# Performance work log

Hardware: AMD Instinct MI355X
Metric: run time of the kernel (lower is better)

Reference implementation:

```python
import jax, jax.numpy as jnp
import numpy as np

L = 32768   # sequence length
H = 256     # dim_ssm_io
P = 128     # effective state dim = dim_ssm_state // 2 (conj_sym=True)
DT_MIN, DT_MAX = 0.001, 0.1


def setup_inputs() -> dict:
    key = jax.random.key(0)
    kB, kC, kD, kstep, ku = jax.random.split(key, 5)
    n = jnp.arange(P, dtype=jnp.float32)
    # s4d_inv initialization: Lambda = -0.5 + 1j * (P/pi) * (P/(2n+1) - 1)
    Lambda_re = -0.5 * jnp.ones((P,), dtype=jnp.float32)
    Lambda_im = (P / np.pi) * (P / (2.0 * n + 1.0) - 1.0)
    # lecun_normal over fan_in, then / sqrt(2) for conj_sym real/imag split
    B = jax.random.normal(kB, (P, H, 2), dtype=jnp.float32) / jnp.sqrt(2.0 * H)
    C = jax.random.normal(kC, (H, P, 2), dtype=jnp.float32) / jnp.sqrt(2.0 * P)
    D = jax.random.normal(kD, (H,), dtype=jnp.float32)
    log_step = (jax.random.uniform(kstep, (P,), dtype=jnp.float32)
                * (jnp.log(DT_MAX) - jnp.log(DT_MIN)) + jnp.log(DT_MIN))
    input_sequence = jax.random.normal(ku, (L, H), dtype=jnp.float32)
    return {
        "Lambda_re": Lambda_re, "Lambda_im": Lambda_im,
        "B": B, "C": C, "D": D, "log_step": log_step,
        "input_sequence": input_sequence,
    }


def reference(Lambda_re, Lambda_im, B, C, D, log_step, input_sequence):
    # assemble complex params (conj_sym path)
    Lam = Lambda_re + 1j * Lambda_im              # (P,)
    B_tilde = B[..., 0] + 1j * B[..., 1]          # (P, H)
    C_tilde = C[..., 0] + 1j * C[..., 1]          # (H, P)
    step = jnp.exp(log_step)                      # (P,)  step_rescale = 1.0
    # ZOH discretization
    Lambda_bar = jnp.exp(Lam * step)              # (P,)
    B_bar = ((Lambda_bar - 1.0) / Lam)[:, None] * B_tilde  # (P, H)
    # input projection: Bu[l] = B_bar @ u[l]
    Bu = jnp.einsum("lh,ph->lp", input_sequence.astype(B_bar.dtype), B_bar)  # (L, P)
    Lam_elems = jnp.broadcast_to(Lambda_bar, (input_sequence.shape[0], Lambda_bar.shape[0]))

    def lin_op(q_i, q_j):
        A_i, b_i = q_i
        A_j, b_j = q_j
        return (A_j * A_i, A_j * b_i + b_j)

    _, xs = jax.lax.associative_scan(lin_op, (Lam_elems, Bu))  # (L, P) complex
    # output projection with conj symmetry: 2 * Re(C_tilde @ x)
    ys = 2.0 * jnp.einsum("lp,hp->lh", xs, C_tilde).real       # (L, H)
    return ys + D * input_sequence
```

## Files before the change

kernel.cpp:

```cpp
#include <hip/hip_runtime.h>
#include <math.h>

#define L_SEQ   32768
#define H_DIM   256
#define P_DIM   128
#define P2      256
#define NBLK    512
#define ROWS    64
#define TPB     512
#define NSEG    64
#define CPS     8

#define WS_LB    0
#define WS_A64   256
#define WS_A512  512
#define WS_COEF  768
#define WS_APOW  1024
#define WS_E     17408
#define WS_CB    148480
#define WS_PACKS 279552
#define WS_XS    410624
#define WS_S     8799232
#define WS_SC    8815616

typedef __attribute__((ext_vector_type(8))) short short8;
typedef __attribute__((ext_vector_type(4))) float f32x4;

#define SAK 264
#define STL 260

__device__ __forceinline__ void split_bf16(float v, ushort& hi, ushort& lo) {
    union { float f; unsigned u; } a; a.f = v;
    unsigned r = a.u + 0x7FFFu + ((a.u >> 16) & 1u);
    hi = (ushort)(r >> 16);
    union { unsigned u; float f; } hf; hf.u = ((unsigned)hi) << 16;
    float rem = v - hf.f;
    union { float f; unsigned u; } b; b.f = rem;
    unsigned r2 = b.u + 0x7FFFu + ((b.u >> 16) & 1u);
    lo = (ushort)(r2 >> 16);
}

__device__ __forceinline__ void split_bf16_fast(float v, ushort& hi, ushort& lo) {
    union { float f; unsigned u; } a; a.f = v;
    hi = (ushort)(a.u >> 16);
    union { unsigned u; float f; } hf; hf.u = a.u & 0xFFFF0000u;
    float rem = v - hf.f;
    union { float f; unsigned u; } b; b.f = rem;
    unsigned r2 = b.u + 0x7FFFu + ((b.u >> 16) & 1u);
    lo = (ushort)(r2 >> 16);
}

__device__ __forceinline__ float4 cfma2(const float4 A, const float4 x, const float4 f) {
    float4 o;
    o.x = A.x * x.x - A.y * x.y + f.x;
    o.y = A.x * x.y + A.y * x.x + f.y;
    o.z = A.z * x.z - A.w * x.w + f.z;
    o.w = A.z * x.w + A.w * x.z + f.w;
    return o;
}

__global__ void k_setup_p(const float* __restrict__ lre, const float* __restrict__ lim,
                          const float* __restrict__ lstep, float* __restrict__ ws) {
    int p = threadIdx.x;
    if (p >= P_DIM) return;
    float step = expf(lstep[p]);
    float lr = lre[p], li = lim[p];
    double zd = (double)lr * (double)step;
    double yd = (double)li * (double)step;
    double ed = exp(zd), cd = cos(yd), sd = sin(yd);
    double lbr = ed * cd, lbi = ed * sd;
    ws[WS_LB + 2*p]     = (float)lbr;
    ws[WS_LB + 2*p + 1] = (float)lbi;
    double mr = lbr, mi = lbi;
    ws[WS_APOW + 2*p]     = (float)mr;
    ws[WS_APOW + 2*p + 1] = (float)mi;
    for (int i = 1; i < 64; i++) {
        double nr = mr * lbr - mi * lbi;
        mi = mr * lbi + mi * lbr;
        mr = nr;
        ws[WS_APOW + i*P2 + 2*p]     = (float)mr;
        ws[WS_APOW + i*P2 + 2*p + 1] = (float)mi;
    }
    ws[WS_A64 + 2*p]     = (float)mr;
    ws[WS_A64 + 2*p + 1] = (float)mi;
    double ar = mr, ai = mi;
    for (int j = 0; j < 3; j++) {
        double nr = ar*ar - ai*ai;
        ai = 2.0 * ar * ai;
        ar = nr;
    }
    ws[WS_A512 + 2*p]     = (float)ar;
    ws[WS_A512 + 2*p + 1] = (float)ai;
    float lbrf = (float)lbr, lbif = (float)lbi;
    float a = lbrf - 1.0f, b = lbif;
    float den = lr*lr + li*li;
    ws[WS_COEF + 2*p]     = (a*lr + b*li) / den;
    ws[WS_COEF + 2*p + 1] = (b*lr - a*li) / den;
}

__global__ void k_setup_mats(const float* __restrict__ B, const float* __restrict__ C,
                             const float* __restrict__ coef,
                             ushort* __restrict__ w1h, ushort* __restrict__ w1l,
                             ushort* __restrict__ w2h, ushort* __restrict__ w2l) {
    int t = blockIdx.x * blockDim.x + threadIdx.x;
    for (int e = t; e < P_DIM * H_DIM; e += 64 * 256) {
        int p = e >> 8;
        int h = e & 255;
        float br = B[(size_t)(p*H_DIM + h)*2 + 0];
        float bi = B[(size_t)(p*H_DIM + h)*2 + 1];
        float cr = coef[2*p], ci = coef[2*p + 1];
        float v1r = cr*br - ci*bi;
        float v1i = cr*bi + ci*br;
        ushort hi, lo;
        split_bf16(v1r, hi, lo);
        w1h[(size_t)(2*p)*256 + h] = hi;  w1l[(size_t)(2*p)*256 + h] = lo;
        split_bf16(v1i, hi, lo);
        w1h[(size_t)(2*p+1)*256 + h] = hi; w1l[(size_t)(2*p+1)*256 + h] = lo;
        float Cr = C[(size_t)(h*P_DIM + p)*2 + 0];
        float Ci = C[(size_t)(h*P_DIM + p)*2 + 1];
        split_bf16(2.0f*Cr, hi, lo);
        w2h[(size_t)h*256 + 2*p] = hi;    w2l[(size_t)h*256 + 2*p] = lo;
        split_bf16(-2.0f*Ci, hi, lo);
        w2h[(size_t)h*256 + 2*p+1] = hi;  w2l[(size_t)h*256 + 2*p+1] = lo;
    }
}

__global__ void k_carry_reduce(const float* __restrict__ E, float* __restrict__ S,
                               const float* __restrict__ a64) {
    const int s = blockIdx.x;
    const int q = threadIdx.x;
    const float4 A = *(const float4*)(a64 + 4 * q);
    const float* xe = E + (size_t)s * CPS * P2 + 4 * q;
    float4 e = make_float4(0.f, 0.f, 0.f, 0.f);
    #pragma unroll
    for (int j = 0; j < CPS; j++)
        e = cfma2(A, e, *(const float4*)(xe + (size_t)j * P2));
    *(float4*)(S + (size_t)s * P2 + 4 * q) = e;
}

__global__ void k_carry_scan(const float* __restrict__ S, float* __restrict__ SC,
                             const float* __restrict__ a512) {
    const int q = threadIdx.x;
    const float4 AS = *(const float4*)(a512 + 4 * q);
    float4 c = make_float4(0.f, 0.f, 0.f, 0.f);
    #pragma unroll 8
    for (int s = 0; s < NSEG; s++) {
        *(float4*)(SC + (size_t)s * P2 + 4 * q) = c;
        c = cfma2(AS, c, *(const float4*)(S + (size_t)s * P2 + 4 * q));
    }
}

__global__ void k_carry_apply(const float* __restrict__ E, const float* __restrict__ SC,
                              float* __restrict__ cb, const float* __restrict__ a64) {
    const int s = blockIdx.x;
    const int q = threadIdx.x;
    const float4 A = *(const float4*)(a64 + 4 * q);
    const float* xe = E + (size_t)s * CPS * P2 + 4 * q;
    float* cw = cb + (size_t)s * CPS * P2 + 4 * q;
    float4 c = *(const float4*)(SC + (size_t)s * P2 + 4 * q);
    #pragma unroll
    for (int j = 0; j < CPS; j++) {
        *(float4*)(cw + (size_t)j * P2) = c;
        c = cfma2(A, c, *(const float4*)(xe + (size_t)j * P2));
    }
}

template<bool EPI, bool APPLY, bool SCAN, bool BSPLIT>
__global__ __launch_bounds__(TPB, 4) void k_gemm_mfma(
        const float* __restrict__ A, const ushort* __restrict__ Wh,
        const ushort* __restrict__ Wl, float* __restrict__ Cmat,
        const float* __restrict__ Dv, const float* __restrict__ U,
        const float* __restrict__ ws, float* __restrict__ Eout,
        const float* __restrict__ cbin) {
    __shared__ float4 SMraw[4224];
    ushort* Ah   = (ushort*)SMraw;
    ushort* Al   = Ah + ROWS * SAK;
    float*  Tile = (float*)SMraw;

    const int t      = threadIdx.x;
    const int lane   = t & 63;
    const int wave   = t >> 6;
    const int lane16 = lane & 15;
    const int quad   = lane >> 4;
    const int blk    = blockIdx.x;
    const int l0     = blk * ROWS;

    {
        float4 f[8];
        #pragma unroll
        for (int j = 0; j < 8; j++)
            f[j] = *(const float4*)(A + (size_t)(l0 + j*8 + wave) * 256 + lane * 4);
        if (APPLY) {
            const float4 cr = *(const float4*)(cbin + (size_t)blk * P2 + lane * 4);
            #pragma unroll
            for (int j = 0; j < 8; j++) {
                const float4 ap = *(const float4*)(ws + WS_APOW + (size_t)(j*8 + wave) * P2 + lane * 4);
                f[j] = cfma2(ap, cr, f[j]);
            }
        }
        #pragma unroll
        for (int j = 0; j < 8; j++) {
            const int m = j*8 + wave;
            ushort4 h4, l4;
            split_bf16_fast(f[j].x, h4.x, l4.x);
            split_bf16_fast(f[j].y, h4.y, l4.y);
            split_bf16_fast(f[j].z, h4.z, l4.z);
            split_bf16_fast(f[j].w, h4.w, l4.w);
            *(ushort4*)(&Ah[m * SAK + lane * 4]) = h4;
            *(ushort4*)(&Al[m * SAK + lane * 4]) = l4;
        }
    }
    __syncthreads();

    f32x4 acc[4][2];
    #pragma unroll
    for (int i = 0; i < 4; i++)
        #pragma unroll
        for (int j = 0; j < 2; j++) acc[i][j] = (f32x4){0.f, 0.f, 0.f, 0.f};

    const ushort* WhB = Wh + (size_t)(wave * 32 + lane16) * 256 + quad * 8;
    const ushort* WlB = Wl + (size_t)(wave * 32 + lane16) * 256 + quad * 8;

    #pragma unroll
    for (int kt = 0; kt < 8; kt++) {
        const int k0 = kt * 32;
        short8 ah[4], alo[4];
        #pragma unroll
        for (int mf = 0; mf < 4; mf++) {
            int m = mf * 16 + lane16;
            ah[mf]  = *(const short8*)(&Ah[m * SAK + k0 + quad * 8]);
            alo[mf] = *(const short8*)(&Al[m * SAK + k0 + quad * 8]);
        }
        #pragma unroll
        for (int nf = 0; nf < 2; nf++) {
            short8 bh = *(const short8*)(WhB + (size_t)nf * 4096 + k0);
            short8 bl;
            if (BSPLIT) bl = *(const short8*)(WlB + (size_t)nf * 4096 + k0);
            #pragma unroll
            for (int mf = 0; mf < 4; mf++) {
                acc[mf][nf] = __builtin_amdgcn_mfma_f32_16x16x32_bf16(ah[mf],  bh, acc[mf][nf], 0, 0, 0);
                if (BSPLIT)
                    acc[mf][nf] = __builtin_amdgcn_mfma_f32_16x16x32_bf16(ah[mf], bl, acc[mf][nf], 0, 0, 0);
                acc[mf][nf] = __builtin_amdgcn_mfma_f32_16x16x32_bf16(alo[mf], bh, acc[mf][nf], 0, 0, 0);
            }
        }
    }

    __syncthreads();
    #pragma unroll
    for (int mf = 0; mf < 4; mf++)
        #pragma unroll
        for (int nf = 0; nf < 2; nf++) {
            int row = mf * 16 + quad * 4;
            int col = wave * 32 + nf * 16 + lane16;
            #pragma unroll
            for (int r = 0; r < 4; r++)
                Tile[(row + r) * STL + col] = acc[mf][nf][r];
        }
    __syncthreads();

    if (!SCAN) {
        const float4 dv = *(const float4*)(Dv + 4 * lane);
        #pragma unroll
        for (int r = 0; r < 8; r++) {
            const int row = wave * 8 + r;
            const float4 tv = *(const float4*)(Tile + row * STL + 4 * lane);
            float4 y = tv;
            if (EPI) {
                const float4 uv = *(const float4*)(U + (size_t)(l0 + row) * 256 + 4 * lane);
                y.x += dv.x * uv.x;  y.y += dv.y * uv.y;
                y.z += dv.z * uv.z;  y.w += dv.w * uv.w;
            }
            *(float4*)(Cmat + (size_t)(l0 + row) * 256 + 4 * lane) = y;
        }
    } else {
        const float4 Alb = *(const float4*)(ws + WS_LB + 4 * lane);
        const float* Trow = Tile + (wave * 8) * STL + 4 * lane;
        float4 v[8];
        float4 x = make_float4(0.f, 0.f, 0.f, 0.f);
        #pragma unroll
        for (int r = 0; r < 8; r++) {
            x = cfma2(Alb, x, *(const float4*)(Trow + r * STL));
            v[r] = x;
        }
        __syncthreads();
        *(float4*)(Tile + wave * STL + 4 * lane) = v[7];
        __syncthreads();
        if (wave == 0) {
            const float4 A8 = *(const float4*)(ws + WS_APOW + 7 * P2 + 4 * lane);
            float4 c = make_float4(0.f, 0.f, 0.f, 0.f);
            #pragma unroll
            for (int j = 0; j < 8; j++) {
                const float4 s = *(const float4*)(Tile + j * STL + 4 * lane);
                *(float4*)(Tile + (8 + j) * STL + 4 * lane) = c;
                c = cfma2(A8, c, s);
            }
        }
        __syncthreads();
        const float4 c = *(const float4*)(Tile + (8 + wave) * STL + 4 * lane);
        float* gbase = Cmat + (size_t)(l0 + wave * 8) * 256 + 4 * lane;
        #pragma unroll
        for (int r = 0; r < 8; r++) {
            const float4 ap = *(const float4*)(ws + WS_APOW + (size_t)r * P2 + 4 * lane);
            const float4 y = cfma2(ap, c, v[r]);
            *(float4*)(gbase + (size_t)r * 256) = y;
            if (r == 7 && wave == 7)
                *(float4*)(Eout + (size_t)blk * P2 + 4 * lane) = y;
        }
    }
}

extern "C" void kernel_launch(void* const* d_in, const int* in_sizes, int n_in,
                              void* d_out, int out_size, void* d_ws, size_t ws_size,
                              hipStream_t stream) {
    const float* lre   = (const float*)d_in[0];
    const float* lim   = (const float*)d_in[1];
    const float* B     = (const float*)d_in[2];
    const float* C     = (const float*)d_in[3];
    const float* D     = (const float*)d_in[4];
    const float* lstep = (const float*)d_in[5];
    const float* u     = (const float*)d_in[6];
    float* out = (float*)d_out;
    float* ws  = (float*)d_ws;
    float* xs  = ws + WS_XS;
    ushort* wpk = (ushort*)(ws + WS_PACKS);
    ushort* w1h = wpk;
    ushort* w1l = wpk + 65536;
    ushort* w2h = wpk + 131072;
    ushort* w2l = wpk + 196608;

    k_setup_p<<<1, 128, 0, stream>>>(lre, lim, lstep, ws);
    k_setup_mats<<<64, 256, 0, stream>>>(B, C, ws + WS_COEF, w1h, w1l, w2h, w2l);
    k_gemm_mfma<false, false, true, true><<<NBLK, TPB, 0, stream>>>(
        u, w1h, w1l, xs, nullptr, nullptr, ws, ws + WS_E, nullptr);
    k_carry_reduce<<<NSEG, 64, 0, stream>>>(ws + WS_E, ws + WS_S, ws + WS_A64);
    k_carry_scan<<<1, 64, 0, stream>>>(ws + WS_S, ws + WS_SC, ws + WS_A512);
    k_carry_apply<<<NSEG, 64, 0, stream>>>(ws + WS_E, ws + WS_SC, ws + WS_CB,
                                           ws + WS_A64);
    k_gemm_mfma<true, true, false, false><<<NBLK, TPB, 0, stream>>>(
        xs, w2h, w2l, out, D, u, ws, nullptr, ws + WS_CB);
}
```

Before: 149.4 us.

## Fold carry scan into second GEMM and store intermediate states as bf16

Drops the three carry kernels (reduce, scan, apply). Each block of the second GEMM now computes its own incoming carry: its 8 waves each walk a strided subset of the preceding block-end states with precomputed powers of Lambda, and the partial results are summed through shared memory. The intermediate state tensor is written and read as bf16 instead of fp32, and the second GEMM uses a single bf16 operand pass with a direct epilogue, cutting launches and memory traffic. In exchange there is redundant carry work per block (up to 64 sequential steps per wave for late blocks) and lower precision in the output projection.

```diff
diff --git a/kernel.cpp b/kernel.cpp
--- a/kernel.cpp
+++ b/kernel.cpp
@@ -8,20 +8,16 @@
 #define NBLK    512
 #define ROWS    64
 #define TPB     512
-#define NSEG    64
-#define CPS     8
+#define NW      8
 
 #define WS_LB    0
-#define WS_A64   256
-#define WS_A512  512
-#define WS_COEF  768
-#define WS_APOW  1024
-#define WS_E     17408
-#define WS_CB    148480
-#define WS_PACKS 279552
-#define WS_XS    410624
-#define WS_S     8799232
-#define WS_SC    8815616
+#define WS_A64P  256
+#define WS_A512  2304
+#define WS_COEF  2560
+#define WS_APOW  2816
+#define WS_E     19200
+#define WS_PACKS 150272
+#define WS_XS16  248576
 
 typedef __attribute__((ext_vector_type(8))) short short8;
 typedef __attribute__((ext_vector_type(4))) float f32x4;
@@ -48,6 +44,16 @@
     union { float f; unsigned u; } b; b.f = rem;
     unsigned r2 = b.u + 0x7FFFu + ((b.u >> 16) & 1u);
     lo = (ushort)(r2 >> 16);
+}
+
+__device__ __forceinline__ ushort rne_bf16(float v) {
+    union { float f; unsigned u; } a; a.f = v;
+    return (ushort)((a.u + 0x7FFFu + ((a.u >> 16) & 1u)) >> 16);
+}
+
+__device__ __forceinline__ float bf16_to_f32(ushort h) {
+    union { unsigned u; float f; } b; b.u = ((unsigned)h) << 16;
+    return b.f;
 }
 
 __device__ __forceinline__ float4 cfma2(const float4 A, const float4 x, const float4 f) {
@@ -81,16 +87,20 @@
         ws[WS_APOW + i*P2 + 2*p]     = (float)mr;
         ws[WS_APOW + i*P2 + 2*p + 1] = (float)mi;
     }
-    ws[WS_A64 + 2*p]     = (float)mr;
-    ws[WS_A64 + 2*p + 1] = (float)mi;
-    double ar = mr, ai = mi;
-    for (int j = 0; j < 3; j++) {
-        double nr = ar*ar - ai*ai;
-        ai = 2.0 * ar * ai;
+    double ar = 1.0, ai = 0.0;
+    ws[WS_A64P + 2*p]     = 1.0f;
+    ws[WS_A64P + 2*p + 1] = 0.0f;
+    for (int d = 1; d < 8; d++) {
+        double nr = ar * mr - ai * mi;
+        ai = ar * mi + ai * mr;
         ar = nr;
-    }
-    ws[WS_A512 + 2*p]     = (float)ar;
-    ws[WS_A512 + 2*p + 1] = (float)ai;
+        ws[WS_A64P + d*P2 + 2*p]     = (float)ar;
+        ws[WS_A64P + d*P2 + 2*p + 1] = (float)ai;
+    }
+    double tr = ar * mr - ai * mi;
+    double ti = ar * mi + ai * mr;
+    ws[WS_A512 + 2*p]     = (float)tr;
+    ws[WS_A512 + 2*p + 1] = (float)ti;
     float lbrf = (float)lbr, lbif = (float)lbi;
     float a = lbrf - 1.0f, b = lbif;
     float den = lr*lr + li*li;
@@ -101,7 +111,7 @@
 __global__ void k_setup_mats(const float* __restrict__ B, const float* __restrict__ C,
                              const float* __restrict__ coef,
                              ushort* __restrict__ w1h, ushort* __restrict__ w1l,
-                             ushort* __restrict__ w2h, ushort* __restrict__ w2l) {
+                             ushort* __restrict__ w2h) {
     int t = blockIdx.x * blockDim.x + threadIdx.x;
     for (int e = t; e < P_DIM * H_DIM; e += 64 * 256) {
         int p = e >> 8;
@@ -119,59 +129,16 @@
         float Cr = C[(size_t)(h*P_DIM + p)*2 + 0];
         float Ci = C[(size_t)(h*P_DIM + p)*2 + 1];
         split_bf16(2.0f*Cr, hi, lo);
-        w2h[(size_t)h*256 + 2*p] = hi;    w2l[(size_t)h*256 + 2*p] = lo;
+        w2h[(size_t)h*256 + 2*p] = hi;
         split_bf16(-2.0f*Ci, hi, lo);
-        w2h[(size_t)h*256 + 2*p+1] = hi;  w2l[(size_t)h*256 + 2*p+1] = lo;
-    }
-}
-
-__global__ void k_carry_reduce(const float* __restrict__ E, float* __restrict__ S,
-                               const float* __restrict__ a64) {
-    const int s = blockIdx.x;
-    const int q = threadIdx.x;
-    const float4 A = *(const float4*)(a64 + 4 * q);
-    const float* xe = E + (size_t)s * CPS * P2 + 4 * q;
-    float4 e = make_float4(0.f, 0.f, 0.f, 0.f);
-    #pragma unroll
-    for (int j = 0; j < CPS; j++)
-        e = cfma2(A, e, *(const float4*)(xe + (size_t)j * P2));
-    *(float4*)(S + (size_t)s * P2 + 4 * q) = e;
-}
-
-__global__ void k_carry_scan(const float* __restrict__ S, float* __restrict__ SC,
-                             const float* __restrict__ a512) {
-    const int q = threadIdx.x;
-    const float4 AS = *(const float4*)(a512 + 4 * q);
-    float4 c = make_float4(0.f, 0.f, 0.f, 0.f);
-    #pragma unroll 8
-    for (int s = 0; s < NSEG; s++) {
-        *(float4*)(SC + (size_t)s * P2 + 4 * q) = c;
-        c = cfma2(AS, c, *(const float4*)(S + (size_t)s * P2 + 4 * q));
-    }
-}
-
-__global__ void k_carry_apply(const float* __restrict__ E, const float* __restrict__ SC,
-                              float* __restrict__ cb, const float* __restrict__ a64) {
-    const int s = blockIdx.x;
-    const int q = threadIdx.x;
-    const float4 A = *(const float4*)(a64 + 4 * q);
-    const float* xe = E + (size_t)s * CPS * P2 + 4 * q;
-    float* cw = cb + (size_t)s * CPS * P2 + 4 * q;
-    float4 c = *(const float4*)(SC + (size_t)s * P2 + 4 * q);
-    #pragma unroll
-    for (int j = 0; j < CPS; j++) {
-        *(float4*)(cw + (size_t)j * P2) = c;
-        c = cfma2(A, c, *(const float4*)(xe + (size_t)j * P2));
-    }
-}
-
-template<bool EPI, bool APPLY, bool SCAN, bool BSPLIT>
-__global__ __launch_bounds__(TPB, 4) void k_gemm_mfma(
-        const float* __restrict__ A, const ushort* __restrict__ Wh,
-        const ushort* __restrict__ Wl, float* __restrict__ Cmat,
-        const float* __restrict__ Dv, const float* __restrict__ U,
-        const float* __restrict__ ws, float* __restrict__ Eout,
-        const float* __restrict__ cbin) {
+        w2h[(size_t)h*256 + 2*p+1] = hi;
+    }
+}
+
+__global__ __launch_bounds__(TPB, 4) void k_gemm1(
+        const float* __restrict__ u, const ushort* __restrict__ Wh,
+        const ushort* __restrict__ Wl, ushort* __restrict__ xs16,
+        const float* __restrict__ ws, float* __restrict__ E) {
     __shared__ float4 SMraw[4224];
     ushort* Ah   = (ushort*)SMraw;
     ushort* Al   = Ah + ROWS * SAK;
@@ -189,15 +156,7 @@
         float4 f[8];
         #pragma unroll
         for (int j = 0; j < 8; j++)
-            f[j] = *(const float4*)(A + (size_t)(l0 + j*8 + wave) * 256 + lane * 4);
-        if (APPLY) {
-            const float4 cr = *(const float4*)(cbin + (size_t)blk * P2 + lane * 4);
-            #pragma unroll
-            for (int j = 0; j < 8; j++) {
-                const float4 ap = *(const float4*)(ws + WS_APOW + (size_t)(j*8 + wave) * P2 + lane * 4);
-                f[j] = cfma2(ap, cr, f[j]);
-            }
-        }
+            f[j] = *(const float4*)(u + (size_t)(l0 + j*8 + wave) * 256 + lane * 4);
         #pragma unroll
         for (int j = 0; j < 8; j++) {
             const int m = j*8 + wave;
@@ -234,13 +193,11 @@
         #pragma unroll
         for (int nf = 0; nf < 2; nf++) {
             short8 bh = *(const short8*)(WhB + (size_t)nf * 4096 + k0);
-            short8 bl;
-            if (BSPLIT) bl = *(const short8*)(WlB + (size_t)nf * 4096 + k0);
+            short8 bl = *(const short8*)(WlB + (size_t)nf * 4096 + k0);
             #pragma unroll
             for (int mf = 0; mf < 4; mf++) {
                 acc[mf][nf] = __builtin_amdgcn_mfma_f32_16x16x32_bf16(ah[mf],  bh, acc[mf][nf], 0, 0, 0);
-                if (BSPLIT)
-                    acc[mf][nf] = __builtin_amdgcn_mfma_f32_16x16x32_bf16(ah[mf], bl, acc[mf][nf], 0, 0, 0);
+                acc[mf][nf] = __builtin_amdgcn_mfma_f32_16x16x32_bf16(ah[mf],  bl, acc[mf][nf], 0, 0, 0);
                 acc[mf][nf] = __builtin_amdgcn_mfma_f32_16x16x32_bf16(alo[mf], bh, acc[mf][nf], 0, 0, 0);
             }
         }
@@ -259,53 +216,145 @@
         }
     __syncthreads();
 
-    if (!SCAN) {
-        const float4 dv = *(const float4*)(Dv + 4 * lane);
-        #pragma unroll
-        for (int r = 0; r < 8; r++) {
-            const int row = wave * 8 + r;
-            const float4 tv = *(const float4*)(Tile + row * STL + 4 * lane);
-            float4 y = tv;
-            if (EPI) {
-                const float4 uv = *(const float4*)(U + (size_t)(l0 + row) * 256 + 4 * lane);
-                y.x += dv.x * uv.x;  y.y += dv.y * uv.y;
-                y.z += dv.z * uv.z;  y.w += dv.w * uv.w;
-            }
-            *(float4*)(Cmat + (size_t)(l0 + row) * 256 + 4 * lane) = y;
-        }
-    } else {
-        const float4 Alb = *(const float4*)(ws + WS_LB + 4 * lane);
+    const float4 Alb = *(const float4*)(ws + WS_LB + 4 * lane);
+    float4 v[8];
+    {
         const float* Trow = Tile + (wave * 8) * STL + 4 * lane;
-        float4 v[8];
         float4 x = make_float4(0.f, 0.f, 0.f, 0.f);
         #pragma unroll
         for (int r = 0; r < 8; r++) {
             x = cfma2(Alb, x, *(const float4*)(Trow + r * STL));
             v[r] = x;
         }
+    }
+    __syncthreads();
+    *(float4*)(Tile + wave * STL + 4 * lane) = v[7];
+    __syncthreads();
+    if (wave == 0) {
+        const float4 A8 = *(const float4*)(ws + WS_APOW + 7 * P2 + 4 * lane);
+        float4 c = make_float4(0.f, 0.f, 0.f, 0.f);
+        #pragma unroll
+        for (int j = 0; j < 8; j++) {
+            const float4 s = *(const float4*)(Tile + j * STL + 4 * lane);
+            *(float4*)(Tile + (8 + j) * STL + 4 * lane) = c;
+            c = cfma2(A8, c, s);
+        }
+    }
+    __syncthreads();
+    const float4 cs = *(const float4*)(Tile + (8 + wave) * STL + 4 * lane);
+    ushort* g16 = xs16 + (size_t)(l0 + wave * 8) * 256 + 4 * lane;
+    #pragma unroll
+    for (int r = 0; r < 8; r++) {
+        const float4 ap = *(const float4*)(ws + WS_APOW + (size_t)r * P2 + 4 * lane);
+        const float4 y = cfma2(ap, cs, v[r]);
+        ushort4 q;
+        q.x = rne_bf16(y.x);  q.y = rne_bf16(y.y);
+        q.z = rne_bf16(y.z);  q.w = rne_bf16(y.w);
+        *(ushort4*)(g16 + (size_t)r * 256) = q;
+        if (r == 7 && wave == 7)
+            *(float4*)(E + (size_t)blk * P2 + 4 * lane) = y;
+    }
+}
+
+__global__ __launch_bounds__(TPB, 4) void k_gemm2(
+        const ushort* __restrict__ xs16, const ushort* __restrict__ w2h,
+        float* __restrict__ out, const float* __restrict__ Dv,
+        const float* __restrict__ u, const float* __restrict__ ws,
+        const float* __restrict__ E) {
+    __shared__ ushort Ah[ROWS * SAK];
+    float* Csh = (float*)Ah;
+
+    const int t      = threadIdx.x;
+    const int lane   = t & 63;
+    const int wave   = t >> 6;
+    const int lane16 = lane & 15;
+    const int quad   = lane >> 4;
+    const int blk    = blockIdx.x;
+    const int l0     = blk * ROWS;
+
+    ushort4 xr[8];
+    #pragma unroll
+    for (int j = 0; j < 8; j++)
+        xr[j] = *(const ushort4*)(xs16 + (size_t)(l0 + j*8 + wave) * 256 + 4 * lane);
+
+    float4 c = make_float4(0.f, 0.f, 0.f, 0.f);
+    {
+        float4 p = make_float4(0.f, 0.f, 0.f, 0.f);
+        const int cnt = (blk > wave) ? (((blk - 1 - wave) >> 3) + 1) : 0;
+        if (cnt > 0) {
+            const float4 A5 = *(const float4*)(ws + WS_A512 + 4 * lane);
+            const float* ep = E + (size_t)wave * P2 + 4 * lane;
+            for (int m = 0; m < cnt; m++) {
+                p = cfma2(A5, p, *(const float4*)ep);
+                ep += 8 * P2;
+            }
+            const int jmax = wave + ((cnt - 1) << 3);
+            const int d = blk - 1 - jmax;
+            const float4 Ad = *(const float4*)(ws + WS_A64P + (size_t)d * P2 + 4 * lane);
+            const float4 z = make_float4(0.f, 0.f, 0.f, 0.f);
+            p = cfma2(Ad, p, z);
+        }
+        *(float4*)(Csh + wave * P2 + 4 * lane) = p;
         __syncthreads();
-        *(float4*)(Tile + wave * STL + 4 * lane) = v[7];
+        #pragma unroll
+        for (int w2 = 0; w2 < NW; w2++) {
+            const float4 q = *(const float4*)(Csh + w2 * P2 + 4 * lane);
+            c.x += q.x; c.y += q.y; c.z += q.z; c.w += q.w;
+        }
         __syncthreads();
-        if (wave == 0) {
-            const float4 A8 = *(const float4*)(ws + WS_APOW + 7 * P2 + 4 * lane);
-            float4 c = make_float4(0.f, 0.f, 0.f, 0.f);
+    }
+
+    #pragma unroll
+    for (int j = 0; j < 8; j++) {
+        const int m = j*8 + wave;
+        float4 f;
+        f.x = bf16_to_f32(xr[j].x);  f.y = bf16_to_f32(xr[j].y);
+        f.z = bf16_to_f32(xr[j].z);  f.w = bf16_to_f32(xr[j].w);
+        const float4 ap = *(const float4*)(ws + WS_APOW + (size_t)m * P2 + 4 * lane);
+        f = cfma2(ap, c, f);
+        ushort4 h4;
+        h4.x = rne_bf16(f.x);  h4.y = rne_bf16(f.y);
+        h4.z = rne_bf16(f.z);  h4.w = rne_bf16(f.w);
+        *(ushort4*)(&Ah[m * SAK + lane * 4]) = h4;
+    }
+    __syncthreads();
+
+    f32x4 acc[4][2];
+    #pragma unroll
+    for (int i = 0; i < 4; i++)
+        #pragma unroll
+        for (int j = 0; j < 2; j++) acc[i][j] = (f32x4){0.f, 0.f, 0.f, 0.f};
+
+    const ushort* WB = w2h + (size_t)(wave * 32 + lane16) * 256 + quad * 8;
+
+    #pragma unroll
+    for (int kt = 0; kt < 8; kt++) {
+        const int k0 = kt * 32;
+        short8 ah[4];
+        #pragma unroll
+        for (int mf = 0; mf < 4; mf++)
+            ah[mf] = *(const short8*)(&Ah[(mf * 16 + lane16) * SAK + k0 + quad * 8]);
+        #pragma unroll
+        for (int nf = 0; nf < 2; nf++) {
+            short8 bh = *(const short8*)(WB + (size_t)nf * 4096 + k0);
             #pragma unroll
-            for (int j = 0; j < 8; j++) {
-                const float4 s = *(const float4*)(Tile + j * STL + 4 * lane);
-                *(float4*)(Tile + (8 + j) * STL + 4 * lane) = c;
-                c = cfma2(A8, c, s);
+            for (int mf = 0; mf < 4; mf++)
+                acc[mf][nf] = __builtin_amdgcn_mfma_f32_16x16x32_bf16(ah[mf], bh, acc[mf][nf], 0, 0, 0);
+        }
+    }
+
+    #pragma unroll
+    for (int nf = 0; nf < 2; nf++) {
+        const int col = wave * 32 + nf * 16 + lane16;
+        const float dcol = Dv[col];
+        #pragma unroll
+        for (int mf = 0; mf < 4; mf++) {
+            const int row0 = l0 + mf * 16 + quad * 4;
+            #pragma unroll
+            for (int r = 0; r < 4; r++) {
+                const float uv = u[(size_t)(row0 + r) * 256 + col];
+                out[(size_t)(row0 + r) * 256 + col] = acc[mf][nf][r] + dcol * uv;
             }
-        }
-        __syncthreads();
-        const float4 c = *(const float4*)(Tile + (8 + wave) * STL + 4 * lane);
-        float* gbase = Cmat + (size_t)(l0 + wave * 8) * 256 + 4 * lane;
-        #pragma unroll
-        for (int r = 0; r < 8; r++) {
-            const float4 ap = *(const float4*)(ws + WS_APOW + (size_t)r * P2 + 4 * lane);
-            const float4 y = cfma2(ap, c, v[r]);
-            *(float4*)(gbase + (size_t)r * 256) = y;
-            if (r == 7 && wave == 7)
-                *(float4*)(Eout + (size_t)blk * P2 + 4 * lane) = y;
         }
     }
 }
@@ -322,21 +371,15 @@
     const float* u     = (const float*)d_in[6];
     float* out = (float*)d_out;
     float* ws  = (float*)d_ws;
-    float* xs  = ws + WS_XS;
-    ushort* wpk = (ushort*)(ws + WS_PACKS);
-    ushort* w1h = wpk;
-    ushort* w1l = wpk + 65536;
-    ushort* w2h = wpk + 131072;
-    ushort* w2l = wpk + 196608;
+    ushort* wpk  = (ushort*)(ws + WS_PACKS);
+    ushort* w1h  = wpk;
+    ushort* w1l  = wpk + 65536;
+    ushort* w2h  = wpk + 131072;
+    ushort* xs16 = (ushort*)(ws + WS_XS16);
+    float*  E    = ws + WS_E;
 
     k_setup_p<<<1, 128, 0, stream>>>(lre, lim, lstep, ws);
-    k_setup_mats<<<64, 256, 0, stream>>>(B, C, ws + WS_COEF, w1h, w1l, w2h, w2l);
-    k_gemm_mfma<false, false, true, true><<<NBLK, TPB, 0, stream>>>(
-        u, w1h, w1l, xs, nullptr, nullptr, ws, ws + WS_E, nullptr);
-    k_carry_reduce<<<NSEG, 64, 0, stream>>>(ws + WS_E, ws + WS_S, ws + WS_A64);
-    k_carry_scan<<<1, 64, 0, stream>>>(ws + WS_S, ws + WS_SC, ws + WS_A512);
-    k_carry_apply<<<NSEG, 64, 0, stream>>>(ws + WS_E, ws + WS_SC, ws + WS_CB,
-                                           ws + WS_A64);
-    k_gemm_mfma<true, true, false, false><<<NBLK, TPB, 0, stream>>>(
-        xs, w2h, w2l, out, D, u, ws, nullptr, ws + WS_CB);
-}
+    k_setup_mats<<<64, 256, 0, stream>>>(B, C, ws + WS_COEF, w1h, w1l, w2h);
+    k_gemm1<<<NBLK, TPB, 0, stream>>>(u, w1h, w1l, xs16, ws, E);
+    k_gemm2<<<NBLK, TPB, 0, stream>>>(xs16, w2h, out, D, u, ws, E);
+}
```

After: 147.6 us. Within noise of the previous version (-1.3%).
